# Performance work log

Hardware: AMD Instinct MI355X
Metric: run time of the kernel (lower is better)

The kernel has to match this reference:

```python
import jax, jax.numpy as jnp
import numpy as np

MAX_H = 22
NUM_HEADS = 8
EPS = 1e-5
SLOPE = 0.01  # torch LeakyReLU default


def setup_inputs() -> dict:
    key = jax.random.key(0)
    ks = jax.random.split(key, 8)
    n, c, s, h, w = 16, 64, 30, 64, 22
    cp, v = 64, 17
    p, out_c = 7, 256
    D = c * MAX_H + cp * 2  # fuse_dim = 1536
    sil = jax.random.normal(ks[0], (n, c, s, h, w), dtype=jnp.float32)
    pose = jax.random.normal(ks[1], (n, cp, s, v), dtype=jnp.float32)
    min_idx = jax.random.randint(ks[2], (p, n), 0, h - MAX_H + 1, dtype=jnp.int32)
    max_idx = min_idx + MAX_H  # slices are exactly MAX_H rows (static shape)
    fc_bin = jax.random.normal(ks[3], (p, D, out_c), dtype=jnp.float32) * np.sqrt(2.0 / (D + out_c))
    gamma = 1.0 + 0.1 * jax.random.normal(ks[4], (out_c,), dtype=jnp.float32)
    beta = 0.1 * jax.random.normal(ks[5], (out_c,), dtype=jnp.float32)
    w_qkv = jax.random.normal(ks[6], (3 * out_c, out_c), dtype=jnp.float32) * 0.02
    w_proj = jax.random.normal(ks[7], (out_c, out_c), dtype=jnp.float32) * 0.02
    return {"sil": sil, "pose": pose, "fc_bin": fc_bin, "gamma": gamma, "beta": beta,
            "w_qkv": w_qkv, "w_proj": w_proj, "min_idx": min_idx, "max_idx": max_idx}


def _forward(sil, pose, fc_bin, gamma, beta, w_qkv, w_proj, min_idx):
    n, c, s, h, w = sil.shape
    p = min_idx.shape[0]
    sil_p = jnp.transpose(sil, (0, 2, 1, 3, 4))  # [n,s,c,h,w]
    parts = []
    for j in range(p):  # fixed small part loop; each gather is a big vectorized op
        idx = min_idx[j][:, None] + jnp.arange(MAX_H, dtype=min_idx.dtype)  # [n,MAX_H]
        g = jnp.take_along_axis(sil_p, idx[:, None, None, :, None], axis=3)  # [n,s,c,MAX_H,w]
        parts.append(g.mean(-1) + g.max(-1))  # mean + max pool over width
    silpart = jnp.stack(parts, 0)  # [p,n,s,c,MAX_H]
    silpart = jnp.transpose(silpart, (1, 2, 0, 3, 4)).reshape(n * s, p, c * MAX_H)

    cp, v = pose.shape[1], pose.shape[3]
    pose_r = jnp.transpose(pose, (0, 2, 1, 3)).reshape(n * s, cp, v)  # [ns,cp,17]
    # part 0: AdaptiveAvgPool1d(2) on 5 joints -> mean(j0..j2), mean(j2..j4)
    part0 = jnp.stack([pose_r[:, :, 0:3].mean(-1), pose_r[:, :, 2:5].mean(-1)], -1)  # [ns,cp,2]
    # parts 1..6: pairs of joints, pool(2->2) is identity
    others = pose_r[:, :, 5:].reshape(n * s, cp, 6, 2).transpose(0, 2, 1, 3)  # [ns,6,cp,2]
    posepart = jnp.concatenate([part0[:, None], others], axis=1)  # [ns,p,cp,2]
    posepart = jax.nn.leaky_relu(posepart, SLOPE).reshape(n * s, p, cp * 2)

    fuse = jnp.concatenate([silpart, posepart], axis=2)  # [ns,p,D]
    x = jnp.einsum('npd,pdo->npo', fuse, fc_bin)  # per-part FC -> [ns,p,out]

    # BatchNorm1d (training-mode batch stats) over [ns,out,p]
    x = jnp.transpose(x, (0, 2, 1))  # [ns,out,p]
    mu = x.mean((0, 2), keepdims=True)
    var = x.var((0, 2), keepdims=True)
    x = (x - mu) * jax.lax.rsqrt(var + EPS) * gamma[None, :, None] + beta[None, :, None]
    x = jnp.transpose(x, (0, 2, 1))  # [ns,p,out]

    # Attention over the p part tokens (note: source softmaxes over the HEAD axis)
    B, N, C = x.shape
    hd = C // NUM_HEADS
    qkv = (x @ w_qkv.T).reshape(B, N, 3, NUM_HEADS, hd).transpose(2, 0, 3, 1, 4)
    q, k, vv = qkv[0], qkv[1], qkv[2]  # [B,H,N,hd]
    attn = jnp.einsum('bhnd,bhmd->bhnm', q, k) * (hd ** -0.5)
    attn = jax.nn.softmax(attn, axis=1)  # faithful to attn.softmax(dim=1)
    ao = jnp.einsum('bhnm,bhmd->bhnd', attn, vv).transpose(0, 2, 1, 3).reshape(B, N, C)
    x = x + ao @ w_proj.T

    return x.reshape(n, s, p, C).transpose(0, 3, 1, 2)  # [n,out,s,p]


def reference(sil, pose, fc_bin, gamma, beta, w_qkv, w_proj, min_idx, max_idx):
    # max_idx == min_idx + MAX_H by construction; slice length is static MAX_H
    return _forward(sil, pose, fc_bin, gamma, beta, w_qkv, w_proj, min_idx)
```

## Files before the change

kernel.cpp:

```cpp
#include <hip/hip_runtime.h>
#include <hip/hip_bf16.h>
#include <math.h>

#define NS 480
#define NN 16
#define SS 30
#define CC 64
#define HHH 64
#define WW 22
#define PP 7
#define MAXH 22
#define CP 64
#define VV 17
#define DD 1536
#define OC 256
#define SILD 1408
#define NTOK 3360

typedef __bf16 bf16x8 __attribute__((ext_vector_type(8)));
typedef float f32x4 __attribute__((ext_vector_type(4)));
typedef short short8 __attribute__((ext_vector_type(8)));

__device__ __forceinline__ void gl_lds16(const void* g, void* l) {
    __builtin_amdgcn_global_load_lds(
        (const __attribute__((address_space(1))) void*)g,
        (__attribute__((address_space(3))) void*)l, 16, 0, 0);
}

__device__ __forceinline__ float bf2f(short s) {
    union { float f; unsigned u; } uu; uu.u = ((unsigned)(unsigned short)s) << 16; return uu.f;
}

__global__ __launch_bounds__(256) void prep(const float* __restrict__ sil,
                                            const int* __restrict__ min_idx,
                                            const float* __restrict__ wqkv,
                                            const float* __restrict__ wproj,
                                            const float* __restrict__ fcbin,
                                            const float* __restrict__ pose,
                                            __hip_bfloat16* __restrict__ fuse,
                                            __hip_bfloat16* __restrict__ wqkv16,
                                            __hip_bfloat16* __restrict__ wproj16,
                                            __hip_bfloat16* __restrict__ fcbinT16) {
    __shared__ __align__(16) char smem[47552];
    int b = blockIdx.x, tid = threadIdx.x;
    if (b < 3840) {
        float* lds  = (float*)smem;
        float* hbuf = (float*)(smem + 45056);
        int*   mi_s = (int*)(smem + 47104);
        if (tid < 112) mi_s[tid] = min_idx[tid];
        long long base = (long long)b * 11264;
        int w = tid >> 6, lane = tid & 63;
        const char* gsrc = (const char*)(sil + base) + lane * 16;
        #pragma unroll
        for (int i = 0; i < 11; i++) {
            int ci = w * 11 + i;
            gl_lds16(gsrc + ci * 1024, (char*)smem + ci * 1024);
        }
        __syncthreads();
        #pragma unroll
        for (int rr = 0; rr < 2; rr++) {
            int r = tid + rr * 256;
            const float* row = lds + r * 22;
            float s = 0.f, m = -INFINITY;
            #pragma unroll
            for (int k = 0; k < WW; k++) { float v = row[k]; s += v; m = fmaxf(m, v); }
            hbuf[r] = s * (1.0f / WW) + m;
        }
        __syncthreads();
        int q0 = b * 8;
        for (int idx = tid; idx < 8 * PP * MAXH; idx += 256) {
            int hh = idx % MAXH;
            int t2 = idx / MAXH;
            int j = t2 % PP, qi = t2 / PP;
            int q = q0 + qi;
            int s_i = q % SS, t3 = q / SS;
            int c = t3 & 63, n = t3 >> 6;
            int mi = mi_s[j * NN + n];
            fuse[((long long)(j * NS + n * SS + s_i)) * DD + c * MAXH + hh] =
                __float2bfloat16(hbuf[qi * 64 + mi + hh]);
        }
        return;
    }
    b -= 3840;
    if (b < 768)  { int g = b * 256 + tid; wqkv16[g] = __float2bfloat16(wqkv[g]); return; }
    if (b < 1024) { int g = (b - 768) * 256 + tid; wproj16[g] = __float2bfloat16(wproj[g]); return; }
    if (b < 1696) {
        float (*t)[65] = (float(*)[65])smem;
        int bb = b - 1024;
        int p = bb / 96, r2 = bb % 96, dt = r2 / 4, ot = r2 % 4;
        const float* s = fcbin + ((long long)p * DD + dt * 64) * OC + ot * 64;
        for (int i = tid; i < 64 * 64; i += 256) {
            int r = i >> 6, c = i & 63;
            t[r][c] = s[(long long)r * OC + c];
        }
        __syncthreads();
        __hip_bfloat16* d = fcbinT16 + ((long long)p * OC + ot * 64) * DD + dt * 64;
        for (int i = tid; i < 64 * 64; i += 256) {
            int r = i >> 6, c = i & 63;
            d[(long long)r * DD + c] = __float2bfloat16(t[c][r]);
        }
        return;
    }
    int g = (b - 1696) * 256 + tid;
    int dd = g & 127;
    int t2 = g >> 7;
    int nsi = t2 % NS;
    int j = t2 / NS;
    int n = nsi / SS, s_i = nsi % SS;
    int cpi = dd >> 1, par = dd & 1;
    const float* pr = pose + (((long long)n * CP + cpi) * SS + s_i) * VV;
    float v;
    if (j == 0) {
        v = (par == 0) ? (pr[0] + pr[1] + pr[2]) * (1.f / 3.f)
                       : (pr[2] + pr[3] + pr[4]) * (1.f / 3.f);
    } else {
        v = pr[5 + (j - 1) * 2 + par];
    }
    v = (v > 0.f) ? v : 0.01f * v;
    fuse[(long long)(j * NS + nsi) * DD + SILD + dd] = __float2bfloat16(v);
}

__global__ __launch_bounds__(256) void gemm_fc(
    const __hip_bfloat16* __restrict__ Ain, const __hip_bfloat16* __restrict__ Bt,
    float* __restrict__ Cf, float* __restrict__ partial)
{
    const int M = 480, K = 1536, lda = 1536, ldc = 1792;
    const __hip_bfloat16* Ab = Ain + (long long)blockIdx.z * 480 * 1536;
    const __hip_bfloat16* Bq = Bt + (long long)blockIdx.z * 256 * 1536;
    float* C = Cf + (long long)blockIdx.z * 256;

    __shared__ short As[2][4096];
    __shared__ short Bs[2][4096];
    __shared__ float red[4][2][16][2];

    int tid = threadIdx.x, lane = tid & 63, w = tid >> 6;
    int wm = w >> 1, wn = w & 1;
    int row0 = blockIdx.x * 64, col0 = blockIdx.y * 64;

    f32x4 acc[2][2] = {};
    int nt = K >> 6;

    auto stage = [&](int buf, int k0) {
        int cc = lane & 7;
        #pragma unroll
        for (int i = 0; i < 2; i++) {
            int r = w * 16 + i * 8 + (lane >> 3);
            int grow = row0 + r; if (grow >= M) grow = M - 1;
            const char* ga = (const char*)Ab + (((long long)grow * lda + k0) << 1) + ((cc ^ (r & 7)) << 4);
            gl_lds16(ga, (char*)&As[buf][0] + (w * 16 + i * 8) * 128);
            const char* gb = (const char*)Bq + (((long long)(col0 + r) * K + k0) << 1) + ((cc ^ (r & 7)) << 4);
            gl_lds16(gb, (char*)&Bs[buf][0] + (w * 16 + i * 8) * 128);
        }
    };

    stage(0, 0);
    __syncthreads();
    for (int t = 0; t < nt; t++) {
        int cur = t & 1;
        if (t + 1 < nt) stage(cur ^ 1, (t + 1) << 6);
        #pragma unroll
        for (int ks = 0; ks < 2; ks++) {
            bf16x8 af[2], bfv[2];
            #pragma unroll
            for (int f = 0; f < 2; f++) {
                int r = wm * 32 + f * 16 + (lane & 15);
                int ca = (ks * 4 + (lane >> 4)) ^ (r & 7);
                af[f] = *(const bf16x8*)((const char*)&As[cur][0] + r * 128 + (ca << 4));
                int rb = wn * 32 + f * 16 + (lane & 15);
                int cb = (ks * 4 + (lane >> 4)) ^ (rb & 7);
                bfv[f] = *(const bf16x8*)((const char*)&Bs[cur][0] + rb * 128 + (cb << 4));
            }
            #pragma unroll
            for (int fm = 0; fm < 2; fm++)
                #pragma unroll
                for (int fn = 0; fn < 2; fn++)
                    acc[fm][fn] = __builtin_amdgcn_mfma_f32_16x16x32_bf16(
                        af[fm], bfv[fn], acc[fm][fn], 0, 0, 0);
        }
        __syncthreads();
    }

    float s[2] = {0.f, 0.f}, s2[2] = {0.f, 0.f};
    #pragma unroll
    for (int fm = 0; fm < 2; fm++) {
        #pragma unroll
        for (int fn = 0; fn < 2; fn++) {
            #pragma unroll
            for (int r4 = 0; r4 < 4; r4++) {
                int grow = row0 + wm * 32 + fm * 16 + (lane >> 4) * 4 + r4;
                int gcol = col0 + wn * 32 + fn * 16 + (lane & 15);
                if (grow < M) {
                    float v = acc[fm][fn][r4];
                    C[(long long)grow * ldc + gcol] = v;
                    s[fn] += v; s2[fn] += v * v;
                }
            }
        }
    }
    #pragma unroll
    for (int off = 16; off < 64; off <<= 1) {
        s[0] += __shfl_xor(s[0], off);  s2[0] += __shfl_xor(s2[0], off);
        s[1] += __shfl_xor(s[1], off);  s2[1] += __shfl_xor(s2[1], off);
    }
    if (lane < 16) {
        red[w][0][lane][0] = s[0]; red[w][0][lane][1] = s2[0];
        red[w][1][lane][0] = s[1]; red[w][1][lane][1] = s2[1];
    }
    __syncthreads();
    if (tid < 128) {
        int col = tid >> 1, which = tid & 1;
        int wn2 = (col >> 5) & 1, fn2 = (col >> 4) & 1, c16 = col & 15;
        float v = red[wn2][fn2][c16][which] + red[2 + wn2][fn2][c16][which];
        partial[((long long)(blockIdx.z * 8 + blockIdx.x) * 2 + which) * 256 + blockIdx.y * 64 + col] = v;
    }
}

__global__ __launch_bounds__(256) void qkvattn(const float* __restrict__ xraw,
                                               const __hip_bfloat16* __restrict__ wqkv16,
                                               const __hip_bfloat16* __restrict__ wproj16,
                                               const float* __restrict__ partial,
                                               const float* __restrict__ gamma,
                                               const float* __restrict__ beta,
                                               float* __restrict__ outp) {
    __shared__ short As[16 * 256];
    __shared__ float qkvs[14 * 768];
    __shared__ float as_[2][8][49];
    __shared__ short ao_s[16 * 256];
    __shared__ float Ct[256 * 17];
    __shared__ float ssl[512];

    int tid = threadIdx.x, lane = tid & 63, w = tid >> 6;
    int token0 = blockIdx.x * 14;

    {
        float s = 0.f, s2 = 0.f;
        #pragma unroll 8
        for (int bb = 0; bb < 56; bb++) {
            s  += partial[bb * 512 + tid];
            s2 += partial[bb * 512 + 256 + tid];
        }
        float mu = s * (1.f / NTOK);
        float var = s2 * (1.f / NTOK) - mu * mu;
        float rsig = rsqrtf(var + 1e-5f);
        float sc = gamma[tid] * rsig;
        ssl[tid] = sc;
        ssl[256 + tid] = beta[tid] - mu * sc;
    }
    __syncthreads();

    for (int i = tid; i < 512; i += 256) {
        int r = i >> 5, c8 = i & 31;
        short8 o = {};
        if (r < 14) {
            const float* src = xraw + (long long)(token0 + r) * 256 + c8 * 8;
            float4 v0 = *(const float4*)src;
            float4 v1 = *(const float4*)(src + 4);
            float vv[8] = {v0.x, v0.y, v0.z, v0.w, v1.x, v1.y, v1.z, v1.w};
            #pragma unroll
            for (int j2 = 0; j2 < 8; j2++) {
                float tv = vv[j2] * ssl[c8 * 8 + j2] + ssl[256 + c8 * 8 + j2];
                union { __hip_bfloat16 h; short s; } u; u.h = __float2bfloat16(tv);
                o[j2] = u.s;
            }
        }
        *(short8*)&As[r * 256 + ((c8 ^ (r & 7)) << 3)] = o;
    }
    __syncthreads();

    {
        f32x4 qacc[12] = {};
        int n0w = w * 192;
        #pragma unroll
        for (int k0 = 0; k0 < 256; k0 += 32) {
            int r = lane & 15;
            int kk = k0 + (lane >> 4) * 8;
            int ck = kk >> 3;
            bf16x8 af = *(const bf16x8*)(const void*)&As[r * 256 + ((ck ^ (r & 7)) << 3)];
            #pragma unroll
            for (int fn = 0; fn < 12; fn++) {
                int nn2 = n0w + fn * 16 + (lane & 15);
                bf16x8 bv = *(const bf16x8*)(const void*)((const short*)wqkv16 + nn2 * 256 + kk);
                qacc[fn] = __builtin_amdgcn_mfma_f32_16x16x32_bf16(af, bv, qacc[fn], 0, 0, 0);
            }
        }
        #pragma unroll
        for (int fn = 0; fn < 12; fn++)
            #pragma unroll
            for (int r4 = 0; r4 < 4; r4++) {
                int row = (lane >> 4) * 4 + r4;
                if (row < 14) qkvs[row * 768 + n0w + fn * 16 + (lane & 15)] = qacc[fn][r4];
            }
    }
    __syncthreads();

    for (int t = tid; t < 784; t += 256) {
        int bb = t / 392, r = t % 392, h = r / 49, ij = r % 49, i = ij / 7, j = ij % 7;
        const float* qp = qkvs + (bb * 7 + i) * 768 + h * 32;
        const float* kp = qkvs + (bb * 7 + j) * 768 + 256 + h * 32;
        float acc = 0.f;
        #pragma unroll
        for (int d = 0; d < 32; d++) acc += qp[d] * kp[d];
        as_[bb][h][ij] = acc * 0.17677669529663689f;
    }
    __syncthreads();
    if (tid < 98) {
        int bb = tid / 49, ij = tid % 49;
        float m = -INFINITY;
        #pragma unroll
        for (int h = 0; h < 8; h++) m = fmaxf(m, as_[bb][h][ij]);
        float e[8], sum = 0.f;
        #pragma unroll
        for (int h = 0; h < 8; h++) { e[h] = __expf(as_[bb][h][ij] - m); sum += e[h]; }
        float inv = 1.f / sum;
        #pragma unroll
        for (int h = 0; h < 8; h++) as_[bb][h][ij] = e[h] * inv;
    }
    __syncthreads();
    for (int t = tid; t < 16 * 256; t += 256) {
        int tl = t >> 8, col = t & 255;
        float acc = 0.f;
        if (tl < 14) {
            int bb = tl / 7, i = tl % 7, h = col >> 5;
            const float* ap = &as_[bb][h][i * 7];
            const float* vp = qkvs + (bb * 7) * 768 + 512 + col;
            #pragma unroll
            for (int j = 0; j < 7; j++) acc += ap[j] * vp[j * 768];
        }
        int c16 = col >> 3;
        union { __hip_bfloat16 h2; short s2; } u; u.h2 = __float2bfloat16(acc);
        ao_s[tl * 256 + ((c16 ^ (tl & 7)) << 3) + (col & 7)] = u.s2;
    }
    __syncthreads();
    f32x4 pacc[4] = {};
    int n0 = w * 64;
    #pragma unroll
    for (int k0 = 0; k0 < 256; k0 += 32) {
        int rowa = lane & 15;
        int kk = k0 + (lane >> 4) * 8;
        int c16a = kk >> 3;
        bf16x8 af = *(const bf16x8*)(const void*)&ao_s[rowa * 256 + ((c16a ^ (rowa & 7)) << 3)];
        #pragma unroll
        for (int fn = 0; fn < 4; fn++) {
            int n = n0 + fn * 16 + (lane & 15);
            bf16x8 bfv = *(const bf16x8*)(const void*)((const short*)wproj16 + n * 256 + kk);
            pacc[fn] = __builtin_amdgcn_mfma_f32_16x16x32_bf16(af, bfv, pacc[fn], 0, 0, 0);
        }
    }
    #pragma unroll
    for (int fn = 0; fn < 4; fn++)
        #pragma unroll
        for (int r4 = 0; r4 < 4; r4++) {
            int o = n0 + fn * 16 + (lane & 15);
            int t = (lane >> 4) * 4 + r4;
            Ct[o * 17 + t] = pacc[fn][r4];
        }
    __syncthreads();
    int o = tid;
    int n = token0 / 210, rem0 = token0 % 210;
    float* op = outp + ((long long)(n * 256 + o)) * 210 + rem0;
    float sc = ssl[o], sh = ssl[256 + o];
    #pragma unroll
    for (int t2 = 0; t2 < 14; t2 += 2) {
        float2 v;
        v.x = Ct[o * 17 + t2]     + xraw[(long long)(token0 + t2) * 256 + o] * sc + sh;
        v.y = Ct[o * 17 + t2 + 1] + xraw[(long long)(token0 + t2 + 1) * 256 + o] * sc + sh;
        *(float2*)(op + t2) = v;
    }
}

extern "C" void kernel_launch(void* const* d_in, const int* in_sizes, int n_in,
                              void* d_out, int out_size, void* d_ws, size_t ws_size,
                              hipStream_t stream) {
    const float* sil   = (const float*)d_in[0];
    const float* pose  = (const float*)d_in[1];
    const float* fcbin = (const float*)d_in[2];
    const float* gamma = (const float*)d_in[3];
    const float* beta  = (const float*)d_in[4];
    const float* wqkv  = (const float*)d_in[5];
    const float* wproj = (const float*)d_in[6];
    const int*   minidx= (const int*)d_in[7];
    float* out = (float*)d_out;

    float* ws = (float*)d_ws;
    __hip_bfloat16* fuse16   = (__hip_bfloat16*)ws;
    float* xraw    = ws + 2580480;
    float* partial = ws + 3440640;
    __hip_bfloat16* wqkv16   = (__hip_bfloat16*)(ws + 3469312);
    __hip_bfloat16* wproj16  = (__hip_bfloat16*)(ws + 3567616);
    __hip_bfloat16* fcbinT16 = (__hip_bfloat16*)(ws + 3600384);

    prep<<<7216, 256, 0, stream>>>(sil, minidx, wqkv, wproj, fcbin, pose,
                                   fuse16, wqkv16, wproj16, fcbinT16);
    gemm_fc<<<dim3(8, 4, 7), 256, 0, stream>>>(fuse16, fcbinT16, xraw, partial);
    qkvattn<<<240, 256, 0, stream>>>(xraw, wqkv16, wproj16, partial, gamma, beta, out);
}
```

Measured before the change: 84.65 us.

## Split K across two wave groups in gemm_fc with LDS reduction

The fc GEMM now launches 512 threads per block, where two groups of four waves each take half of the K dimension (768). The partial accumulators are then reduced through LDS before the output and BN statistics are written. The grid has only 224 blocks, so this aims to put more waves in flight and shorten each block's serial K loop. In exchange it doubles LDS use per block and adds a barrier plus the LDS round-trip for the reduction.

Result: faster. 81.32 us (-3.9%).

```diff
diff --git a/kernel.cpp b/kernel.cpp
--- a/kernel.cpp
+++ b/kernel.cpp
@@ -120,7 +120,7 @@
     fuse[(long long)(j * NS + nsi) * DD + SILD + dd] = __float2bfloat16(v);
 }
 
-__global__ __launch_bounds__(256) void gemm_fc(
+__global__ __launch_bounds__(512) void gemm_fc(
     const __hip_bfloat16* __restrict__ Ain, const __hip_bfloat16* __restrict__ Bt,
     float* __restrict__ Cf, float* __restrict__ partial)
 {
@@ -129,35 +129,37 @@
     const __hip_bfloat16* Bq = Bt + (long long)blockIdx.z * 256 * 1536;
     float* C = Cf + (long long)blockIdx.z * 256;
 
-    __shared__ short As[2][4096];
-    __shared__ short Bs[2][4096];
+    __shared__ short As[2][2][4096];
+    __shared__ short Bs[2][2][4096];
     __shared__ float red[4][2][16][2];
 
     int tid = threadIdx.x, lane = tid & 63, w = tid >> 6;
-    int wm = w >> 1, wn = w & 1;
+    int kg = w >> 2, wq = w & 3;
+    int wm = wq >> 1, wn = wq & 1;
     int row0 = blockIdx.x * 64, col0 = blockIdx.y * 64;
+    int kbase = kg * 768;
 
     f32x4 acc[2][2] = {};
-    int nt = K >> 6;
 
     auto stage = [&](int buf, int k0) {
         int cc = lane & 7;
         #pragma unroll
         for (int i = 0; i < 2; i++) {
-            int r = w * 16 + i * 8 + (lane >> 3);
+            int r = wq * 16 + i * 8 + (lane >> 3);
             int grow = row0 + r; if (grow >= M) grow = M - 1;
-            const char* ga = (const char*)Ab + (((long long)grow * lda + k0) << 1) + ((cc ^ (r & 7)) << 4);
-            gl_lds16(ga, (char*)&As[buf][0] + (w * 16 + i * 8) * 128);
-            const char* gb = (const char*)Bq + (((long long)(col0 + r) * K + k0) << 1) + ((cc ^ (r & 7)) << 4);
-            gl_lds16(gb, (char*)&Bs[buf][0] + (w * 16 + i * 8) * 128);
+            long long kk = kbase + k0;
+            const char* ga = (const char*)Ab + (((long long)grow * lda + kk) << 1) + ((cc ^ (r & 7)) << 4);
+            gl_lds16(ga, (char*)&As[kg][buf][0] + (wq * 16 + i * 8) * 128);
+            const char* gb = (const char*)Bq + (((long long)(col0 + r) * K + kk) << 1) + ((cc ^ (r & 7)) << 4);
+            gl_lds16(gb, (char*)&Bs[kg][buf][0] + (wq * 16 + i * 8) * 128);
         }
     };
 
     stage(0, 0);
     __syncthreads();
-    for (int t = 0; t < nt; t++) {
+    for (int t = 0; t < 12; t++) {
         int cur = t & 1;
-        if (t + 1 < nt) stage(cur ^ 1, (t + 1) << 6);
+        if (t + 1 < 12) stage(cur ^ 1, (t + 1) << 6);
         #pragma unroll
         for (int ks = 0; ks < 2; ks++) {
             bf16x8 af[2], bfv[2];
@@ -165,10 +167,10 @@
             for (int f = 0; f < 2; f++) {
                 int r = wm * 32 + f * 16 + (lane & 15);
                 int ca = (ks * 4 + (lane >> 4)) ^ (r & 7);
-                af[f] = *(const bf16x8*)((const char*)&As[cur][0] + r * 128 + (ca << 4));
+                af[f] = *(const bf16x8*)((const char*)&As[kg][cur][0] + r * 128 + (ca << 4));
                 int rb = wn * 32 + f * 16 + (lane & 15);
                 int cb = (ks * 4 + (lane >> 4)) ^ (rb & 7);
-                bfv[f] = *(const bf16x8*)((const char*)&Bs[cur][0] + rb * 128 + (cb << 4));
+                bfv[f] = *(const bf16x8*)((const char*)&Bs[kg][cur][0] + rb * 128 + (cb << 4));
             }
             #pragma unroll
             for (int fm = 0; fm < 2; fm++)
@@ -180,31 +182,49 @@
         __syncthreads();
     }
 
-    float s[2] = {0.f, 0.f}, s2[2] = {0.f, 0.f};
-    #pragma unroll
-    for (int fm = 0; fm < 2; fm++) {
-        #pragma unroll
-        for (int fn = 0; fn < 2; fn++) {
-            #pragma unroll
-            for (int r4 = 0; r4 < 4; r4++) {
-                int grow = row0 + wm * 32 + fm * 16 + (lane >> 4) * 4 + r4;
-                int gcol = col0 + wn * 32 + fn * 16 + (lane & 15);
-                if (grow < M) {
-                    float v = acc[fm][fn][r4];
-                    C[(long long)grow * ldc + gcol] = v;
-                    s[fn] += v; s2[fn] += v * v;
+    float* redC = (float*)&As[0][0][0];
+    if (kg == 1) {
+        #pragma unroll
+        for (int fm = 0; fm < 2; fm++)
+            #pragma unroll
+            for (int fn = 0; fn < 2; fn++)
+                #pragma unroll
+                for (int r4 = 0; r4 < 4; r4++) {
+                    int rl = wm * 32 + fm * 16 + (lane >> 4) * 4 + r4;
+                    int cl = wn * 32 + fn * 16 + (lane & 15);
+                    redC[rl * 64 + cl] = acc[fm][fn][r4];
+                }
+    }
+    __syncthreads();
+
+    if (kg == 0) {
+        float s[2] = {0.f, 0.f}, s2[2] = {0.f, 0.f};
+        #pragma unroll
+        for (int fm = 0; fm < 2; fm++) {
+            #pragma unroll
+            for (int fn = 0; fn < 2; fn++) {
+                #pragma unroll
+                for (int r4 = 0; r4 < 4; r4++) {
+                    int rl = wm * 32 + fm * 16 + (lane >> 4) * 4 + r4;
+                    int cl = wn * 32 + fn * 16 + (lane & 15);
+                    int grow = row0 + rl;
+                    if (grow < M) {
+                        float v = acc[fm][fn][r4] + redC[rl * 64 + cl];
+                        C[(long long)grow * ldc + col0 + cl] = v;
+                        s[fn] += v; s2[fn] += v * v;
+                    }
                 }
             }
         }
-    }
-    #pragma unroll
-    for (int off = 16; off < 64; off <<= 1) {
-        s[0] += __shfl_xor(s[0], off);  s2[0] += __shfl_xor(s2[0], off);
-        s[1] += __shfl_xor(s[1], off);  s2[1] += __shfl_xor(s2[1], off);
-    }
-    if (lane < 16) {
-        red[w][0][lane][0] = s[0]; red[w][0][lane][1] = s2[0];
-        red[w][1][lane][0] = s[1]; red[w][1][lane][1] = s2[1];
+        #pragma unroll
+        for (int off = 16; off < 64; off <<= 1) {
+            s[0] += __shfl_xor(s[0], off);  s2[0] += __shfl_xor(s2[0], off);
+            s[1] += __shfl_xor(s[1], off);  s2[1] += __shfl_xor(s2[1], off);
+        }
+        if (lane < 16) {
+            red[wq][0][lane][0] = s[0]; red[wq][0][lane][1] = s2[0];
+            red[wq][1][lane][0] = s[1]; red[wq][1][lane][1] = s2[1];
+        }
     }
     __syncthreads();
     if (tid < 128) {
@@ -391,6 +411,6 @@
 
     prep<<<7216, 256, 0, stream>>>(sil, minidx, wqkv, wproj, fcbin, pose,
                                    fuse16, wqkv16, wproj16, fcbinT16);
-    gemm_fc<<<dim3(8, 4, 7), 256, 0, stream>>>(fuse16, fcbinT16, xraw, partial);
+    gemm_fc<<<dim3(8, 4, 7), 512, 0, stream>>>(fuse16, fcbinT16, xraw, partial);
     qkvattn<<<240, 256, 0, stream>>>(xraw, wqkv16, wproj16, partial, gamma, beta, out);
 }
```
